# Kernel tuning notes

Measured on AMD Instinct MI355X. Metric: run time of the kernel, lower is better.

The kernel has to match this reference:

```python
import jax, jax.numpy as jnp
import numpy as np

DIM = 1024
HEADS = 16
D_HEAD = 64
INNER = HEADS * D_HEAD  # 1024
FF_INNER = 4 * DIM      # 4096


def setup_inputs() -> dict:
    key = jax.random.key(0)
    ks = jax.random.split(key, 12)
    s = lambda fan_in: 1.0 / np.sqrt(fan_in)
    x = jax.random.normal(ks[0], (4, 1024, DIM), dtype=jnp.float32)
    context = jax.random.normal(ks[1], (4, 2048, DIM), dtype=jnp.float32)
    Wq = jax.random.normal(ks[2], (DIM, INNER), dtype=jnp.float32) * s(DIM)
    Wk = jax.random.normal(ks[3], (DIM, INNER), dtype=jnp.float32) * s(DIM)
    Wv = jax.random.normal(ks[4], (DIM, INNER), dtype=jnp.float32) * s(DIM)
    Wo = jax.random.normal(ks[5], (INNER, DIM), dtype=jnp.float32) * s(INNER)
    bo = jax.random.normal(ks[6], (DIM,), dtype=jnp.float32) * 0.01
    W1 = jax.random.normal(ks[7], (DIM, FF_INNER), dtype=jnp.float32) * s(DIM)
    b1 = jax.random.normal(ks[8], (FF_INNER,), dtype=jnp.float32) * 0.01
    W2 = jax.random.normal(ks[9], (FF_INNER, DIM), dtype=jnp.float32) * s(FF_INNER)
    b2 = jax.random.normal(ks[10], (DIM,), dtype=jnp.float32) * 0.01
    return {"x": x, "context": context, "Wq": Wq, "Wk": Wk, "Wv": Wv,
            "Wo": Wo, "bo": bo, "W1": W1, "b1": b1, "W2": W2, "b2": b2}


def _block(x, context, Wq, Wk, Wv, Wo, bo, W1, b1, W2, b2):
    B, Lq, _ = x.shape
    scale = 1.0 / np.sqrt(D_HEAD).astype(np.float32)
    # cross attention
    q = (x @ Wq).reshape(B, Lq, HEADS, D_HEAD)          # [B,Lq,H,D]
    k = (context @ Wk).reshape(B, -1, HEADS, D_HEAD)    # [B,Lk,H,D]
    v = (context @ Wv).reshape(B, -1, HEADS, D_HEAD)
    sim = jnp.einsum('bqhd,bkhd->bhqk', q, k) * scale   # [B,H,Lq,Lk]
    attn = jax.nn.softmax(sim, axis=-1)
    out = jnp.einsum('bhqk,bkhd->bqhd', attn, v).reshape(B, Lq, INNER)
    x = out @ Wo + bo + x
    # feedforward (exact GELU as in torch F.gelu default)
    h = jax.nn.gelu(x @ W1 + b1, approximate=False)
    return h @ W2 + b2 + x


def reference(x, context, Wq, Wk, Wv, Wo, bo, W1, b1, W2, b2):
    return _block(x, context, Wq, Wk, Wv, Wo, bo, W1, b1, W2, b2)
```

## Files before the change

### kernel.cpp

```cpp
#include <hip/hip_runtime.h>
#include <hip/hip_bf16.h>
#include <cmath>
#include <cstdint>

typedef short s16x8 __attribute__((ext_vector_type(8)));
typedef unsigned short u16x8 __attribute__((ext_vector_type(8)));
typedef unsigned short u16x4 __attribute__((ext_vector_type(4)));
typedef float f32x4 __attribute__((ext_vector_type(4)));

__device__ __forceinline__ float bf2f(uint16_t u) {
  union { uint32_t i; float f; } c; c.i = ((uint32_t)u) << 16; return c.f;
}
__device__ __forceinline__ uint16_t f2bf(float f) {
  union { float f; uint32_t i; } c; c.f = f;
  return (uint16_t)((c.i + 0x7FFFu + ((c.i >> 16) & 1u)) >> 16);
}
__device__ __forceinline__ uint32_t pkbf(float a, float b) {
  union { __hip_bfloat162 h; uint32_t u; } c;
  c.h = __float22bfloat162_rn(float2{a, b});
  return c.u;
}

__device__ __forceinline__ void gload16(const void* g, void* l) {
  __builtin_amdgcn_global_load_lds(
      (const __attribute__((address_space(1))) void*)g,
      (__attribute__((address_space(3))) void*)l, 16, 0, 0);
}

__device__ __forceinline__ bool sniff_is_bf16(const uint16_t* u16, int64_t n,
                                              int tid, int* s_cnt) {
  int cnt = 0;
#pragma unroll
  for (int j = 0; j < 4; j++) {
    int64_t idx = (((int64_t)(tid * 4 + j)) * 2) % n;
    idx &= ~(int64_t)1;
    uint32_t e = (u16[idx] >> 7) & 0xFF;
    cnt += (e >= 96 && e <= 144) ? 1 : 0;
  }
  if (tid == 0) *s_cnt = 0;
  __syncthreads();
  atomicAdd(s_cnt, cnt);
  __syncthreads();
  return (*s_cnt) * 10 > 1024 * 6;
}

__global__ __launch_bounds__(256) void prep_all(
    float* dout,
    const void* xr, const void* cr, const void* bor, const void* b1r, const void* b2r,
    const void* Wq, const void* Wk, const void* Wv, const void* Wo,
    const void* W1, const void* W2,
    uint16_t* xo, uint16_t* co, uint16_t* boo, uint16_t* b1o, uint16_t* b2o,
    uint16_t* WqT, uint16_t* WkT, uint16_t* WvT, uint16_t* WoT,
    uint16_t* W1T, uint16_t* W2T) {
  __shared__ int s_cnt;
  __shared__ uint16_t tile[64][65];
  const int id = blockIdx.x;
  const int tid = threadIdx.x;

  if (id < 1024) {
    float* p = dout + ((int64_t)id * 256 + tid) * 4;
#pragma unroll
    for (int i = 0; i < 4; i++)
      *(f32x4*)(p + (int64_t)i * 262144) = (f32x4){0.f, 0.f, 0.f, 0.f};
    return;
  }
  if (id < 4099) {
    const void* src; uint16_t* dst; int64_t tot; int64_t base; int nv;
    if (id < 2048)      { src = xr; dst = xo; tot = 4194304; base = (int64_t)(id - 1024) * 4096; nv = 4; }
    else if (id < 4096) { src = cr; dst = co; tot = 8388608; base = (int64_t)(id - 2048) * 4096; nv = 4; }
    else if (id == 4096){ src = bor; dst = boo; tot = 1024; base = 0; nv = 1; }
    else if (id == 4097){ src = b1r; dst = b1o; tot = 4096; base = 0; nv = 4; }
    else                { src = b2r; dst = b2o; tot = 1024; base = 0; nv = 1; }
    const bool is16 = sniff_is_bf16((const uint16_t*)src, tot, tid, &s_cnt);
    if (is16) {
      const uint64_t* s = (const uint64_t*)((const uint16_t*)src + base);
      uint64_t* d = (uint64_t*)(dst + base);
      for (int i = 0; i < nv; i++) d[i * 256 + tid] = s[i * 256 + tid];
    } else {
      const f32x4* s = (const f32x4*)((const float*)src + base);
      uint2* d = (uint2*)(dst + base);
      for (int i = 0; i < nv; i++) {
        f32x4 v = s[i * 256 + tid];
        uint2 o; o.x = pkbf(v[0], v[1]); o.y = pkbf(v[2], v[3]);
        d[i * 256 + tid] = o;
      }
    }
    return;
  }
  const int t0 = id - 4099;
  const void* src; uint16_t* dst; int R, C, bx, by;
  if (t0 < 1024) {
    const int wsel = t0 >> 8, t = t0 & 255;
    const void* srcs[4] = {Wq, Wk, Wv, Wo};
    uint16_t* dsts[4] = {WqT, WkT, WvT, WoT};
    src = srcs[wsel]; dst = dsts[wsel]; R = 1024; C = 1024; bx = t & 15; by = t >> 4;
  } else if (t0 < 2048) { int t = t0 - 1024; src = W1; dst = W1T; R = 1024; C = 4096; bx = t & 63; by = t >> 6; }
  else                  { int t = t0 - 2048; src = W2; dst = W2T; R = 4096; C = 1024; bx = t & 15; by = t >> 4; }
  const uint16_t* u16 = (const uint16_t*)src;
  const float* f32 = (const float*)src;
  const bool is16 = sniff_is_bf16(u16, (int64_t)R * C, tid, &s_cnt);
  const int c0 = bx * 64, r0 = by * 64;
  if (is16) {
    const int c8 = (tid & 7) * 8, r = tid >> 3;
#pragma unroll
    for (int ri = 0; ri < 2; ri++) {
      const int row = r + ri * 32;
      u16x8 v = *(const u16x8*)(u16 + (int64_t)(r0 + row) * C + c0 + c8);
#pragma unroll
      for (int j = 0; j < 8; j++) tile[c8 + j][row] = v[j];
    }
  } else {
    const int c4 = (tid & 15) * 4, r = tid >> 4;
#pragma unroll
    for (int ri = 0; ri < 4; ri++) {
      const int row = r + ri * 16;
      f32x4 v = *(const f32x4*)(f32 + (int64_t)(r0 + row) * C + c0 + c4);
#pragma unroll
      for (int j = 0; j < 4; j++) tile[c4 + j][row] = f2bf(v[j]);
    }
  }
  __syncthreads();
  const int rr8 = (tid & 7) * 8, cc = tid >> 3;
#pragma unroll
  for (int ci = 0; ci < 2; ci++) {
    const int col = cc + ci * 32;
    *(u16x8*)(dst + (int64_t)(c0 + col) * R + r0 + rr8) = *(const u16x8*)&tile[col][rr8];
  }
}

__global__ __launch_bounds__(256) void vtrans(
    const uint16_t* __restrict__ KVb, uint16_t* __restrict__ Vt) {
  __shared__ uint16_t tile[64][65];
  const int z = blockIdx.z;
  const uint16_t* in = KVb + (int64_t)z * 2048 * 2048 + 1024;
  uint16_t* out = Vt + (int64_t)z * 1024 * 2048;
  const int tid = threadIdx.x;
  const int c0 = blockIdx.x * 64, k0 = blockIdx.y * 64;
  const int c8 = (tid & 7) * 8, r = tid >> 3;
#pragma unroll
  for (int ri = 0; ri < 2; ri++) {
    const int krow = r + ri * 32;
    u16x8 v = *(const u16x8*)(in + (int64_t)(k0 + krow) * 2048 + c0 + c8);
#pragma unroll
    for (int j = 0; j < 8; j++) tile[c8 + j][krow] = v[j];
  }
  __syncthreads();
  const int k8 = (tid & 7) * 8, cc = tid >> 3;
#pragma unroll
  for (int ci = 0; ci < 2; ci++) {
    const int col = cc + ci * 32;
    *(u16x8*)(out + (int64_t)(c0 + col) * 2048 + k0 + k8) = *(const u16x8*)&tile[col][k8];
  }
}

#define BM 128
#define BN 128
#define BK 64

enum { EPI_NONE = 0, EPI_BIAS_RES = 1, EPI_BIAS_GELU = 2 };

template <int EPI, int RESF32, int OUTF32, int SPLITK>
__device__ __forceinline__ void gemm_body(
    const uint16_t* __restrict__ A, const uint16_t* __restrict__ Bt,
    void* __restrict__ Cv, const uint16_t* __restrict__ bias,
    const void* __restrict__ resid, int M, int N, int K_total,
    int m0, int n0, int zslice, uint16_t* As, uint16_t* Bs) {
  const int tid = threadIdx.x;
  const int w = tid >> 6, l = tid & 63;
  const int wu = __builtin_amdgcn_readfirstlane(w);
  const int wm = (w >> 1) * 64, wn = (w & 1) * 64;
  const int ls = l & 15, lg = l >> 4;
  const int K = SPLITK ? (K_total >> 1) : K_total;
  const int kof = SPLITK ? zslice * K : 0;

  const int sr = 8 * w + (l >> 3);
  const int koff = (((l & 7) ^ ((l >> 3) & 7)) * 8);
  const uint16_t* Ag = A + (int64_t)(m0 + sr) * K_total + kof + koff;
  const uint16_t* Bg = Bt + (int64_t)(n0 + sr) * K_total + kof + koff;
  const int64_t rstep = (int64_t)32 * K_total;

  uint16_t* lA = As + wu * 512;
  uint16_t* lB = Bs + wu * 512;

  f32x4 acc[4][4] = {};

  for (int kb = 0; kb < K; kb += BK) {
    __syncthreads();
#pragma unroll
    for (int r = 0; r < 4; r++) {
      gload16(Ag + r * rstep + kb, lA + r * 2048);
      gload16(Bg + r * rstep + kb, lB + r * 2048);
    }
    __syncthreads();
#pragma unroll
    for (int kk = 0; kk < 2; kk++) {
      s16x8 af[4], bfr[4];
#pragma unroll
      for (int i = 0; i < 4; i++) {
        const int row = wm + i * 16 + ls;
        af[i] = *(const s16x8*)&As[row * 64 + (((kk * 4 + lg) ^ (ls & 7)) * 8)];
      }
#pragma unroll
      for (int j = 0; j < 4; j++) {
        const int row = wn + j * 16 + ls;
        bfr[j] = *(const s16x8*)&Bs[row * 64 + (((kk * 4 + lg) ^ (ls & 7)) * 8)];
      }
#pragma unroll
      for (int i = 0; i < 4; i++)
#pragma unroll
        for (int j = 0; j < 4; j++)
          acc[i][j] = __builtin_amdgcn_mfma_f32_16x16x32_bf16(af[i], bfr[j], acc[i][j], 0, 0, 0);
    }
  }

#pragma unroll
  for (int i = 0; i < 4; i++) {
#pragma unroll
    for (int rr = 0; rr < 4; rr++) {
      const int64_t row = m0 + wm + i * 16 + lg * 4 + rr;
#pragma unroll
      for (int j = 0; j < 4; j++) {
        const int col = n0 + wn + j * 16 + ls;
        float v = acc[i][j][rr];
        if (EPI == EPI_BIAS_RES) {
          if (!SPLITK || zslice == 0) {
            const float rv = RESF32 ? ((const float*)resid)[row * N + col]
                                    : bf2f(((const uint16_t*)resid)[row * N + col]);
            v += bf2f(bias[col]) + rv;
          }
        } else if (EPI == EPI_BIAS_GELU) {
          v += bf2f(bias[col]);
          v = 0.5f * v * (1.0f + erff(v * 0.70710678118654752f));
        }
        if (SPLITK)
          atomicAdd((float*)Cv + row * N + col, v);
        else if (OUTF32)
          ((float*)Cv)[row * N + col] = v;
        else
          ((uint16_t*)Cv)[row * N + col] = f2bf(v);
      }
    }
  }
}

template <int EPI, int RESF32, int OUTF32, int SPLITK>
__global__ __launch_bounds__(256, 3) void gemm_single(
    const uint16_t* __restrict__ A, const uint16_t* __restrict__ Bt,
    void* __restrict__ Cv, const uint16_t* __restrict__ bias,
    const void* __restrict__ resid, int M, int N, int K_total) {
  __shared__ alignas(16) uint16_t As[BM * BK];
  __shared__ alignas(16) uint16_t Bs[BN * BK];
  gemm_body<EPI, RESF32, OUTF32, SPLITK>(A, Bt, Cv, bias, resid, M, N, K_total,
                                         blockIdx.x * BM, blockIdx.y * BN,
                                         (int)blockIdx.z, As, Bs);
}

__global__ __launch_bounds__(256, 3) void gemm_qkv(
    const uint16_t* __restrict__ xA, const uint16_t* __restrict__ WqT,
    uint16_t* __restrict__ Qb,
    const uint16_t* __restrict__ ctxA, const uint16_t* __restrict__ KVWt,
    uint16_t* __restrict__ KVb) {
  __shared__ alignas(16) uint16_t As[BM * BK];
  __shared__ alignas(16) uint16_t Bs[BN * BK];
  const int id = blockIdx.x;
  if (id < 256) {
    gemm_body<EPI_NONE, 0, 0, 0>(xA, WqT, Qb, nullptr, nullptr, 4096, 1024, 1024,
                                 (id & 31) * BM, (id >> 5) * BN, 0, As, Bs);
  } else {
    const int t = id - 256;
    gemm_body<EPI_NONE, 0, 0, 0>(ctxA, KVWt, KVb, nullptr, nullptr, 8192, 2048, 1024,
                                 (t & 63) * BM, (t >> 6) * BN, 0, As, Bs);
  }
}

#define KLD 72
#define PLD 72

__global__ __launch_bounds__(256, 2) void attn_kernel(
    const uint16_t* __restrict__ Q,
    const uint16_t* __restrict__ KV,
    const uint16_t* __restrict__ Vt,
    uint16_t* __restrict__ O) {
  __shared__ alignas(16) uint16_t Ks[64 * KLD];
  __shared__ alignas(16) uint16_t Vts[64 * KLD];
  __shared__ alignas(16) uint16_t Ps[8][16 * PLD];

  const int tid = threadIdx.x;
  const int w = tid >> 6, l = tid & 63;
  const int ls = l & 15, lg = l >> 4;

  const int blk = blockIdx.x;
  const int bh = blk & 63;
  const int qb = blk >> 6;
  const int h = bh & 15, b = bh >> 4;

  const int64_t qrow0 = (int64_t)b * 1024 + qb * 128;
  const int hoff = h * 64;
  const uint16_t* Vtb = Vt + (int64_t)b * 1024 * 2048;

  const float sc = 0.125f * 1.4426950408889634f;

  s16x8 qf[2][2];
#pragma unroll
  for (int qq = 0; qq < 2; qq++)
#pragma unroll
    for (int ks = 0; ks < 2; ks++) {
      s16x8 r = *(const s16x8*)(Q + (qrow0 + w * 32 + qq * 16 + ls) * 1024 + hoff + ks * 32 + lg * 8);
#pragma unroll
      for (int j = 0; j < 8; j++)
        qf[qq][ks][j] = (short)f2bf(bf2f((uint16_t)r[j]) * sc);
    }

  f32x4 oacc[2][4] = {};
  float lsum[2] = {0.f, 0.f};

  const int srow = tid >> 3;
  const int sc8 = (tid & 7) * 8;
  const uint16_t* Kg = KV + ((int64_t)b * 2048 + srow) * 2048 + hoff + sc8;
  const uint16_t* Vg = Vtb + (int64_t)(hoff + srow) * 2048 + sc8;

  s16x8 rk0 = *(const s16x8*)(Kg);
  s16x8 rk1 = *(const s16x8*)(Kg + (int64_t)32 * 2048);
  s16x8 rv0 = *(const s16x8*)(Vg);
  s16x8 rv1 = *(const s16x8*)(Vg + (int64_t)32 * 2048);

  for (int kt = 0; kt < 2048; kt += 64) {
    __syncthreads();
    *(s16x8*)&Ks[srow * KLD + sc8] = rk0;
    *(s16x8*)&Ks[(srow + 32) * KLD + sc8] = rk1;
    *(s16x8*)&Vts[srow * KLD + sc8] = rv0;
    *(s16x8*)&Vts[(srow + 32) * KLD + sc8] = rv1;
    const int ktn = kt + 64;
    if (ktn < 2048) {
      rk0 = *(const s16x8*)(Kg + (int64_t)ktn * 2048);
      rk1 = *(const s16x8*)(Kg + (int64_t)(ktn + 32) * 2048);
      rv0 = *(const s16x8*)(Vg + ktn);
      rv1 = *(const s16x8*)(Vg + ktn + (int64_t)32 * 2048);
    }
    __syncthreads();

    f32x4 st[2][4];
#pragma unroll
    for (int jn = 0; jn < 4; jn++) {
      f32x4 z = {0.f, 0.f, 0.f, 0.f};
      st[0][jn] = z; st[1][jn] = z;
#pragma unroll
      for (int ks = 0; ks < 2; ks++) {
        s16x8 kf = *(const s16x8*)&Ks[(jn * 16 + ls) * KLD + ks * 32 + lg * 8];
        st[0][jn] = __builtin_amdgcn_mfma_f32_16x16x32_bf16(kf, qf[0][ks], st[0][jn], 0, 0, 0);
        st[1][jn] = __builtin_amdgcn_mfma_f32_16x16x32_bf16(kf, qf[1][ks], st[1][jn], 0, 0, 0);
      }
    }

#pragma unroll
    for (int qq = 0; qq < 2; qq++)
#pragma unroll
      for (int jn = 0; jn < 4; jn++) {
        const float p0 = exp2f(st[qq][jn][0]);
        const float p1 = exp2f(st[qq][jn][1]);
        const float p2 = exp2f(st[qq][jn][2]);
        const float p3 = exp2f(st[qq][jn][3]);
        lsum[qq] += (p0 + p1) + (p2 + p3);
        uint2 pk; pk.x = pkbf(p0, p1); pk.y = pkbf(p2, p3);
        *(uint2*)&Ps[w * 2 + qq][ls * PLD + jn * 16 + lg * 4] = pk;
      }

#pragma unroll
    for (int ks = 0; ks < 2; ks++) {
      s16x8 pf0 = *(const s16x8*)&Ps[w * 2 + 0][ls * PLD + ks * 32 + lg * 8];
      s16x8 pf1 = *(const s16x8*)&Ps[w * 2 + 1][ls * PLD + ks * 32 + lg * 8];
#pragma unroll
      for (int jn = 0; jn < 4; jn++) {
        s16x8 vf = *(const s16x8*)&Vts[(jn * 16 + ls) * KLD + ks * 32 + lg * 8];
        oacc[0][jn] = __builtin_amdgcn_mfma_f32_16x16x32_bf16(pf0, vf, oacc[0][jn], 0, 0, 0);
        oacc[1][jn] = __builtin_amdgcn_mfma_f32_16x16x32_bf16(pf1, vf, oacc[1][jn], 0, 0, 0);
      }
    }
  }

#pragma unroll
  for (int qq = 0; qq < 2; qq++) {
    float red = lsum[qq];
    red += __shfl_xor(red, 16, 64);
    red += __shfl_xor(red, 32, 64);
#pragma unroll
    for (int rr = 0; rr < 4; rr++) {
      const float inv = 1.0f / __shfl(red, lg * 4 + rr, 64);
      const int64_t row = qrow0 + w * 32 + qq * 16 + lg * 4 + rr;
#pragma unroll
      for (int jn = 0; jn < 4; jn++)
        O[row * 1024 + hoff + jn * 16 + ls] = f2bf(oacc[qq][jn][rr] * inv);
    }
  }
}

extern "C" void kernel_launch(void* const* d_in, const int* in_sizes, int n_in,
                              void* d_out, int out_size, void* d_ws, size_t ws_size,
                              hipStream_t stream) {
  const void* x_raw   = d_in[0];
  const void* ctx_raw = d_in[1];
  const void* Wq_raw  = d_in[2];
  const void* Wk_raw  = d_in[3];
  const void* Wv_raw  = d_in[4];
  const void* Wo_raw  = d_in[5];
  const void* bo_raw  = d_in[6];
  const void* W1_raw  = d_in[7];
  const void* b1_raw  = d_in[8];
  const void* W2_raw  = d_in[9];
  const void* b2_raw  = d_in[10];

  const int64_t Mi = 1 << 20;
  uint16_t* ws   = (uint16_t*)d_ws;
  uint16_t* WqT  = ws;
  uint16_t* KVWt = ws + 1 * Mi;
  uint16_t* WoT  = ws + 3 * Mi;
  uint16_t* W1T  = ws + 4 * Mi;
  uint16_t* W2T  = ws + 8 * Mi;
  uint16_t* bob  = ws + 12 * Mi;
  uint16_t* b1b  = ws + 12 * Mi + 1024;
  uint16_t* b2b  = ws + 12 * Mi + 5120;
  uint16_t* xb   = ws + 13 * Mi;
  uint16_t* AO   = ws + 13 * Mi;
  uint16_t* ctxb = ws + 17 * Mi;
  uint16_t* Vt   = ws + 17 * Mi;
  uint16_t* X1   = ws + 17 * Mi;
  uint16_t* Qb   = ws + 25 * Mi;
  uint16_t* KVb  = ws + 29 * Mi;
  uint16_t* Hb   = ws + 29 * Mi;

  const dim3 tb(256);
  prep_all<<<dim3(7171), tb, 0, stream>>>(
      (float*)d_out,
      x_raw, ctx_raw, bo_raw, b1_raw, b2_raw,
      Wq_raw, Wk_raw, Wv_raw, Wo_raw, W1_raw, W2_raw,
      xb, ctxb, bob, b1b, b2b,
      WqT, KVWt, KVWt + Mi, WoT, W1T, W2T);

  gemm_qkv<<<dim3(1280), tb, 0, stream>>>(xb, WqT, Qb, ctxb, KVWt, KVb);

  vtrans<<<dim3(16, 32, 4), tb, 0, stream>>>(KVb, Vt);

  attn_kernel<<<dim3(512), tb, 0, stream>>>(Qb, KVb, Vt, AO);

  gemm_single<EPI_BIAS_RES, 1, 0, 0><<<dim3(32, 8), tb, 0, stream>>>(
      AO, WoT, X1, bob, x_raw, 4096, 1024, 1024);
  gemm_single<EPI_BIAS_GELU, 0, 0, 0><<<dim3(32, 32), tb, 0, stream>>>(
      X1, W1T, Hb, b1b, nullptr, 4096, 4096, 1024);
  gemm_single<EPI_BIAS_RES, 0, 1, 1><<<dim3(32, 8, 2), tb, 0, stream>>>(
      Hb, W2T, d_out, b2b, X1, 4096, 1024, 4096);
}
```

Before: 400.8 us.

## Stage GEMM epilogues through LDS, replace split-K atomics, load attention K/V directly

GEMM epilogues now write accumulators to shared memory and emit coalesced vector stores. The exact erf in the GELU epilogue is replaced by a polynomial erf approximation. The FF2 split-K drops the output zeroing and atomicAdds: each slice writes its own fp32 partial, and a new reduce kernel sums them with bias and residual. The attention kernel drops LDS staging of K and V and loads fragments straight from global memory into registers, which removes barriers but adds uncached global traffic. The erf approximation changes GELU numerics slightly.

```diff
diff --git a/kernel.cpp b/kernel.cpp
--- a/kernel.cpp
+++ b/kernel.cpp
@@ -19,6 +19,18 @@
   union { __hip_bfloat162 h; uint32_t u; } c;
   c.h = __float22bfloat162_rn(float2{a, b});
   return c.u;
+}
+
+__device__ __forceinline__ float gelu_exactf(float v) {
+  const float x = v * 0.70710678118654752f;
+  const float ax = fabsf(x);
+  const float t = 1.0f / (1.0f + 0.3275911f * ax);
+  const float poly = ((((1.061405429f * t - 1.453152027f) * t + 1.421413741f) * t
+                      - 0.284496736f) * t + 0.254829592f) * t;
+  const float e = __expf(-x * x);
+  float er = 1.0f - poly * e;
+  er = copysignf(er, x);
+  return 0.5f * v * (1.0f + er);
 }
 
 __device__ __forceinline__ void gload16(const void* g, void* l) {
@@ -45,7 +57,6 @@
 }
 
 __global__ __launch_bounds__(256) void prep_all(
-    float* dout,
     const void* xr, const void* cr, const void* bor, const void* b1r, const void* b2r,
     const void* Wq, const void* Wk, const void* Wv, const void* Wo,
     const void* W1, const void* W2,
@@ -57,19 +68,12 @@
   const int id = blockIdx.x;
   const int tid = threadIdx.x;
 
-  if (id < 1024) {
-    float* p = dout + ((int64_t)id * 256 + tid) * 4;
-#pragma unroll
-    for (int i = 0; i < 4; i++)
-      *(f32x4*)(p + (int64_t)i * 262144) = (f32x4){0.f, 0.f, 0.f, 0.f};
-    return;
-  }
-  if (id < 4099) {
+  if (id < 3075) {
     const void* src; uint16_t* dst; int64_t tot; int64_t base; int nv;
-    if (id < 2048)      { src = xr; dst = xo; tot = 4194304; base = (int64_t)(id - 1024) * 4096; nv = 4; }
-    else if (id < 4096) { src = cr; dst = co; tot = 8388608; base = (int64_t)(id - 2048) * 4096; nv = 4; }
-    else if (id == 4096){ src = bor; dst = boo; tot = 1024; base = 0; nv = 1; }
-    else if (id == 4097){ src = b1r; dst = b1o; tot = 4096; base = 0; nv = 4; }
+    if (id < 1024)      { src = xr; dst = xo; tot = 4194304; base = (int64_t)id * 4096; nv = 4; }
+    else if (id < 3072) { src = cr; dst = co; tot = 8388608; base = (int64_t)(id - 1024) * 4096; nv = 4; }
+    else if (id == 3072){ src = bor; dst = boo; tot = 1024; base = 0; nv = 1; }
+    else if (id == 3073){ src = b1r; dst = b1o; tot = 4096; base = 0; nv = 4; }
     else                { src = b2r; dst = b2o; tot = 1024; base = 0; nv = 1; }
     const bool is16 = sniff_is_bf16((const uint16_t*)src, tot, tid, &s_cnt);
     if (is16) {
@@ -87,7 +91,7 @@
     }
     return;
   }
-  const int t0 = id - 4099;
+  const int t0 = id - 3075;
   const void* src; uint16_t* dst; int R, C, bx, by;
   if (t0 < 1024) {
     const int wsel = t0 >> 8, t = t0 & 255;
@@ -153,16 +157,17 @@
   }
 }
 
+enum { EPI_NONE = 0, EPI_BIAS_RES = 1, EPI_BIAS_GELU = 2 };
+
 #define BM 128
 #define BN 128
 #define BK 64
 
-enum { EPI_NONE = 0, EPI_BIAS_RES = 1, EPI_BIAS_GELU = 2 };
-
 template <int EPI, int RESF32, int OUTF32, int SPLITK>
 __device__ __forceinline__ void gemm_body(
     const uint16_t* __restrict__ A, const uint16_t* __restrict__ Bt,
-    void* __restrict__ Cv, const uint16_t* __restrict__ bias,
+    void* __restrict__ Cv, void* __restrict__ Cv2,
+    const uint16_t* __restrict__ bias,
     const void* __restrict__ resid, int M, int N, int K_total,
     int m0, int n0, int zslice, uint16_t* As, uint16_t* Bs) {
   const int tid = threadIdx.x;
@@ -213,32 +218,94 @@
     }
   }
 
-#pragma unroll
-  for (int i = 0; i < 4; i++) {
-#pragma unroll
-    for (int rr = 0; rr < 4; rr++) {
-      const int64_t row = m0 + wm + i * 16 + lg * 4 + rr;
-#pragma unroll
-      for (int j = 0; j < 4; j++) {
-        const int col = n0 + wn + j * 16 + ls;
-        float v = acc[i][j][rr];
-        if (EPI == EPI_BIAS_RES) {
-          if (!SPLITK || zslice == 0) {
-            const float rv = RESF32 ? ((const float*)resid)[row * N + col]
-                                    : bf2f(((const uint16_t*)resid)[row * N + col]);
-            v += bf2f(bias[col]) + rv;
+  constexpr bool F32P = (EPI == EPI_BIAS_RES) || (OUTF32 != 0);
+  if constexpr (F32P) {
+    float* ct = (float*)As;
+    const int er = tid >> 2;
+    const int tg = tid & 3;
+    float* Co = (float*)((SPLITK && zslice) ? Cv2 : Cv);
+#pragma unroll
+    for (int h = 0; h < 2; h++) {
+      __syncthreads();
+      if ((w >> 1) == h) {
+#pragma unroll
+        for (int i = 0; i < 4; i++)
+#pragma unroll
+          for (int rr = 0; rr < 4; rr++) {
+            const int lr = i * 16 + lg * 4 + rr;
+#pragma unroll
+            for (int j = 0; j < 4; j++) {
+              const int c = wn + j * 16 + ls;
+              const int ch = c >> 2;
+              const int pch = (ch & ~7) | ((ch ^ lr) & 7);
+              ct[lr * 128 + pch * 4 + (c & 3)] = acc[i][j][rr];
+            }
           }
-        } else if (EPI == EPI_BIAS_GELU) {
-          v += bf2f(bias[col]);
-          v = 0.5f * v * (1.0f + erff(v * 0.70710678118654752f));
+      }
+      __syncthreads();
+      const int64_t grow = m0 + h * 64 + er;
+      float vr[32];
+#pragma unroll
+      for (int k = 0; k < 8; k++) {
+        const int lch = tg * 8 + k;
+        const int pch = (lch & ~7) | ((lch ^ er) & 7);
+        f32x4 v = *(const f32x4*)&ct[er * 128 + pch * 4];
+#pragma unroll
+        for (int e = 0; e < 4; e++) vr[k * 4 + e] = v[e];
+      }
+      const int c0g = n0 + tg * 32;
+      if (EPI == EPI_BIAS_RES) {
+#pragma unroll
+        for (int k = 0; k < 4; k++) {
+          u16x8 bb = *(const u16x8*)(bias + c0g + k * 8);
+          f32x4 r0 = {}, r1 = {};
+          if (RESF32) {
+            r0 = *(const f32x4*)((const float*)resid + grow * N + (c0g - n0) + n0 + k * 8);
+            r1 = *(const f32x4*)((const float*)resid + grow * N + (c0g - n0) + n0 + k * 8 + 4);
+          }
+          u16x8 o;
+#pragma unroll
+          for (int e = 0; e < 8; e++) {
+            float rv;
+            if (RESF32) rv = (e < 4) ? r0[e] : r1[e - 4];
+            else rv = bf2f(((const uint16_t*)resid)[grow * N + c0g + k * 8 + e]);
+            o[e] = (short)f2bf(vr[k * 8 + e] + bf2f(bb[e]) + rv);
+          }
+          *(u16x8*)(&((uint16_t*)Co)[grow * N + c0g + k * 8]) = o;
         }
-        if (SPLITK)
-          atomicAdd((float*)Cv + row * N + col, v);
-        else if (OUTF32)
-          ((float*)Cv)[row * N + col] = v;
-        else
-          ((uint16_t*)Cv)[row * N + col] = f2bf(v);
-      }
+      } else {
+#pragma unroll
+        for (int k = 0; k < 8; k++)
+          *(f32x4*)(&Co[grow * N + c0g + k * 4]) = *(const f32x4*)&vr[k * 4];
+      }
+    }
+  } else {
+    uint16_t* ctb = As;
+    __syncthreads();
+#pragma unroll
+    for (int i = 0; i < 4; i++)
+#pragma unroll
+      for (int rr = 0; rr < 4; rr++) {
+        const int r = wm + i * 16 + lg * 4 + rr;
+#pragma unroll
+        for (int j = 0; j < 4; j++) {
+          const int c = wn + j * 16 + ls;
+          float v = acc[i][j][rr];
+          if (EPI == EPI_BIAS_GELU) { v += bf2f(bias[n0 + c]); v = gelu_exactf(v); }
+          const int ch = c >> 3;
+          const int pch = (ch & 8) | ((ch ^ r) & 7);
+          ctb[r * 128 + pch * 8 + (c & 7)] = f2bf(v);
+        }
+      }
+    __syncthreads();
+    const int sr2 = tid >> 1, sgb = (tid & 1) * 8;
+    uint16_t* Co16 = (uint16_t*)Cv;
+#pragma unroll
+    for (int k = 0; k < 8; k++) {
+      const int lch = sgb + k;
+      const int pch = (lch & 8) | ((lch ^ sr2) & 7);
+      u16x8 v = *(const u16x8*)&ctb[sr2 * 128 + pch * 8];
+      *(u16x8*)(&Co16[(int64_t)(m0 + sr2) * N + n0 + lch * 8]) = v;
     }
   }
 }
@@ -246,13 +313,13 @@
 template <int EPI, int RESF32, int OUTF32, int SPLITK>
 __global__ __launch_bounds__(256, 3) void gemm_single(
     const uint16_t* __restrict__ A, const uint16_t* __restrict__ Bt,
-    void* __restrict__ Cv, const uint16_t* __restrict__ bias,
+    void* __restrict__ Cv, void* __restrict__ Cv2,
+    const uint16_t* __restrict__ bias,
     const void* __restrict__ resid, int M, int N, int K_total) {
-  __shared__ alignas(16) uint16_t As[BM * BK];
-  __shared__ alignas(16) uint16_t Bs[BN * BK];
-  gemm_body<EPI, RESF32, OUTF32, SPLITK>(A, Bt, Cv, bias, resid, M, N, K_total,
+  __shared__ alignas(16) uint16_t sh[BM * BK + BN * BK];
+  gemm_body<EPI, RESF32, OUTF32, SPLITK>(A, Bt, Cv, Cv2, bias, resid, M, N, K_total,
                                          blockIdx.x * BM, blockIdx.y * BN,
-                                         (int)blockIdx.z, As, Bs);
+                                         (int)blockIdx.z, sh, sh + BM * BK);
 }
 
 __global__ __launch_bounds__(256, 3) void gemm_qkv(
@@ -260,20 +327,36 @@
     uint16_t* __restrict__ Qb,
     const uint16_t* __restrict__ ctxA, const uint16_t* __restrict__ KVWt,
     uint16_t* __restrict__ KVb) {
-  __shared__ alignas(16) uint16_t As[BM * BK];
-  __shared__ alignas(16) uint16_t Bs[BN * BK];
+  __shared__ alignas(16) uint16_t sh[BM * BK + BN * BK];
   const int id = blockIdx.x;
   if (id < 256) {
-    gemm_body<EPI_NONE, 0, 0, 0>(xA, WqT, Qb, nullptr, nullptr, 4096, 1024, 1024,
-                                 (id & 31) * BM, (id >> 5) * BN, 0, As, Bs);
+    gemm_body<EPI_NONE, 0, 0, 0>(xA, WqT, Qb, nullptr, nullptr, nullptr, 4096, 1024, 1024,
+                                 (id & 31) * BM, (id >> 5) * BN, 0, sh, sh + BM * BK);
   } else {
     const int t = id - 256;
-    gemm_body<EPI_NONE, 0, 0, 0>(ctxA, KVWt, KVb, nullptr, nullptr, 8192, 2048, 1024,
-                                 (t & 63) * BM, (t >> 6) * BN, 0, As, Bs);
-  }
-}
-
-#define KLD 72
+    gemm_body<EPI_NONE, 0, 0, 0>(ctxA, KVWt, KVb, nullptr, nullptr, nullptr, 8192, 2048, 1024,
+                                 (t & 63) * BM, (t >> 6) * BN, 0, sh, sh + BM * BK);
+  }
+}
+
+__global__ __launch_bounds__(256) void ff2_reduce(
+    float* __restrict__ dout, const float* __restrict__ p1,
+    const uint16_t* __restrict__ X1, const uint16_t* __restrict__ b2) {
+  const int64_t i0 = ((int64_t)blockIdx.x * 256 + threadIdx.x) * 8;
+  f32x4 d0 = *(const f32x4*)(dout + i0), d1 = *(const f32x4*)(dout + i0 + 4);
+  f32x4 q0 = *(const f32x4*)(p1 + i0),  q1 = *(const f32x4*)(p1 + i0 + 4);
+  u16x8 x = *(const u16x8*)(X1 + i0);
+  u16x8 bb = *(const u16x8*)(b2 + (i0 & 1023));
+  f32x4 r0, r1;
+#pragma unroll
+  for (int e = 0; e < 4; e++) {
+    r0[e] = d0[e] + q0[e] + bf2f(x[e]) + bf2f(bb[e]);
+    r1[e] = d1[e] + q1[e] + bf2f(x[e + 4]) + bf2f(bb[e + 4]);
+  }
+  *(f32x4*)(dout + i0) = r0;
+  *(f32x4*)(dout + i0 + 4) = r1;
+}
+
 #define PLD 72
 
 __global__ __launch_bounds__(256, 2) void attn_kernel(
@@ -281,8 +364,6 @@
     const uint16_t* __restrict__ KV,
     const uint16_t* __restrict__ Vt,
     uint16_t* __restrict__ O) {
-  __shared__ alignas(16) uint16_t Ks[64 * KLD];
-  __shared__ alignas(16) uint16_t Vts[64 * KLD];
   __shared__ alignas(16) uint16_t Ps[8][16 * PLD];
 
   const int tid = threadIdx.x;
@@ -297,6 +378,7 @@
   const int64_t qrow0 = (int64_t)b * 1024 + qb * 128;
   const int hoff = h * 64;
   const uint16_t* Vtb = Vt + (int64_t)b * 1024 * 2048;
+  const uint16_t* Kb = KV + (int64_t)b * 2048 * 2048 + hoff;
 
   const float sc = 0.125f * 1.4426950408889634f;
 
@@ -314,30 +396,13 @@
   f32x4 oacc[2][4] = {};
   float lsum[2] = {0.f, 0.f};
 
-  const int srow = tid >> 3;
-  const int sc8 = (tid & 7) * 8;
-  const uint16_t* Kg = KV + ((int64_t)b * 2048 + srow) * 2048 + hoff + sc8;
-  const uint16_t* Vg = Vtb + (int64_t)(hoff + srow) * 2048 + sc8;
-
-  s16x8 rk0 = *(const s16x8*)(Kg);
-  s16x8 rk1 = *(const s16x8*)(Kg + (int64_t)32 * 2048);
-  s16x8 rv0 = *(const s16x8*)(Vg);
-  s16x8 rv1 = *(const s16x8*)(Vg + (int64_t)32 * 2048);
-
   for (int kt = 0; kt < 2048; kt += 64) {
-    __syncthreads();
-    *(s16x8*)&Ks[srow * KLD + sc8] = rk0;
-    *(s16x8*)&Ks[(srow + 32) * KLD + sc8] = rk1;
-    *(s16x8*)&Vts[srow * KLD + sc8] = rv0;
-    *(s16x8*)&Vts[(srow + 32) * KLD + sc8] = rv1;
-    const int ktn = kt + 64;
-    if (ktn < 2048) {
-      rk0 = *(const s16x8*)(Kg + (int64_t)ktn * 2048);
-      rk1 = *(const s16x8*)(Kg + (int64_t)(ktn + 32) * 2048);
-      rv0 = *(const s16x8*)(Vg + ktn);
-      rv1 = *(const s16x8*)(Vg + ktn + (int64_t)32 * 2048);
-    }
-    __syncthreads();
+    s16x8 kf[4][2];
+#pragma unroll
+    for (int jn = 0; jn < 4; jn++)
+#pragma unroll
+      for (int ks = 0; ks < 2; ks++)
+        kf[jn][ks] = *(const s16x8*)(Kb + (int64_t)(kt + jn * 16 + ls) * 2048 + ks * 32 + lg * 8);
 
     f32x4 st[2][4];
 #pragma unroll
@@ -346,11 +411,17 @@
       st[0][jn] = z; st[1][jn] = z;
 #pragma unroll
       for (int ks = 0; ks < 2; ks++) {
-        s16x8 kf = *(const s16x8*)&Ks[(jn * 16 + ls) * KLD + ks * 32 + lg * 8];
-        st[0][jn] = __builtin_amdgcn_mfma_f32_16x16x32_bf16(kf, qf[0][ks], st[0][jn], 0, 0, 0);
-        st[1][jn] = __builtin_amdgcn_mfma_f32_16x16x32_bf16(kf, qf[1][ks], st[1][jn], 0, 0, 0);
-      }
-    }
+        st[0][jn] = __builtin_amdgcn_mfma_f32_16x16x32_bf16(kf[jn][ks], qf[0][ks], st[0][jn], 0, 0, 0);
+        st[1][jn] = __builtin_amdgcn_mfma_f32_16x16x32_bf16(kf[jn][ks], qf[1][ks], st[1][jn], 0, 0, 0);
+      }
+    }
+
+    s16x8 vf[4][2];
+#pragma unroll
+    for (int jn = 0; jn < 4; jn++)
+#pragma unroll
+      for (int ks = 0; ks < 2; ks++)
+        vf[jn][ks] = *(const s16x8*)(Vtb + (int64_t)(hoff + jn * 16 + ls) * 2048 + kt + ks * 32 + lg * 8);
 
 #pragma unroll
     for (int qq = 0; qq < 2; qq++)
@@ -371,9 +442,8 @@
       s16x8 pf1 = *(const s16x8*)&Ps[w * 2 + 1][ls * PLD + ks * 32 + lg * 8];
 #pragma unroll
       for (int jn = 0; jn < 4; jn++) {
-        s16x8 vf = *(const s16x8*)&Vts[(jn * 16 + ls) * KLD + ks * 32 + lg * 8];
-        oacc[0][jn] = __builtin_amdgcn_mfma_f32_16x16x32_bf16(pf0, vf, oacc[0][jn], 0, 0, 0);
-        oacc[1][jn] = __builtin_amdgcn_mfma_f32_16x16x32_bf16(pf1, vf, oacc[1][jn], 0, 0, 0);
+        oacc[0][jn] = __builtin_amdgcn_mfma_f32_16x16x32_bf16(pf0, vf[jn][ks], oacc[0][jn], 0, 0, 0);
+        oacc[1][jn] = __builtin_amdgcn_mfma_f32_16x16x32_bf16(pf1, vf[jn][ks], oacc[1][jn], 0, 0, 0);
       }
     }
   }
@@ -415,6 +485,7 @@
   uint16_t* KVWt = ws + 1 * Mi;
   uint16_t* WoT  = ws + 3 * Mi;
   uint16_t* W1T  = ws + 4 * Mi;
+  float*    P1f  = (float*)ws;
   uint16_t* W2T  = ws + 8 * Mi;
   uint16_t* bob  = ws + 12 * Mi;
   uint16_t* b1b  = ws + 12 * Mi + 1024;
@@ -429,8 +500,7 @@
   uint16_t* Hb   = ws + 29 * Mi;
 
   const dim3 tb(256);
-  prep_all<<<dim3(7171), tb, 0, stream>>>(
-      (float*)d_out,
+  prep_all<<<dim3(6147), tb, 0, stream>>>(
       x_raw, ctx_raw, bo_raw, b1_raw, b2_raw,
       Wq_raw, Wk_raw, Wv_raw, Wo_raw, W1_raw, W2_raw,
       xb, ctxb, bob, b1b, b2b,
@@ -443,9 +513,10 @@
   attn_kernel<<<dim3(512), tb, 0, stream>>>(Qb, KVb, Vt, AO);
 
   gemm_single<EPI_BIAS_RES, 1, 0, 0><<<dim3(32, 8), tb, 0, stream>>>(
-      AO, WoT, X1, bob, x_raw, 4096, 1024, 1024);
+      AO, WoT, X1, nullptr, bob, x_raw, 4096, 1024, 1024);
   gemm_single<EPI_BIAS_GELU, 0, 0, 0><<<dim3(32, 32), tb, 0, stream>>>(
-      X1, W1T, Hb, b1b, nullptr, 4096, 4096, 1024);
-  gemm_single<EPI_BIAS_RES, 0, 1, 1><<<dim3(32, 8, 2), tb, 0, stream>>>(
-      Hb, W2T, d_out, b2b, X1, 4096, 1024, 4096);
-}
+      X1, W1T, Hb, nullptr, b1b, nullptr, 4096, 4096, 1024);
+  gemm_single<EPI_NONE, 0, 1, 1><<<dim3(32, 8, 2), tb, 0, stream>>>(
+      Hb, W2T, d_out, P1f, nullptr, nullptr, 4096, 1024, 4096);
+  ff2_reduce<<<dim3(2048), tb, 0, stream>>>((float*)d_out, P1f, X1, b2b);
+}
```

Result: slower. 479.6 us (+19.7%).
